# Kernel tuning notes

Hardware: AMD Instinct MI355X
Metric: run time of the kernel (lower is better)

Reference implementation:

```python
import jax, jax.numpy as jnp
import numpy as np

B, SEQ, DIM = 2, 4096, 1024
E, S = 8, 512          # num_slots = seq_len // num_experts
HID = 4 * DIM          # FeedForward hidden: dim * mult
SCALE = DIM ** 0.5     # RMSNorm scale


def rmsnorm(x, gamma):
    # matches F.normalize(x, dim=-1) * dim**0.5 * gamma (eps=1e-12 clamp on the norm)
    n = jnp.linalg.norm(x, axis=-1, keepdims=True)
    return x / jnp.maximum(n, 1e-12) * SCALE * gamma


def setup_inputs() -> dict:
    key = jax.random.key(0)
    ks = jax.random.split(key, 4)
    w_init = lambda k, shape: jax.random.normal(k, shape, dtype=jnp.float32) * 0.02
    return {
        "x": jax.random.normal(ks[0], (B, SEQ, DIM), dtype=jnp.float32),
        "norm_gamma": jnp.ones((DIM,), jnp.float32),
        "slot_norm_gamma": jnp.ones((DIM,), jnp.float32),
        "slot_embeds": jax.random.normal(ks[1], (E, S, DIM), dtype=jnp.float32),
        "w1": w_init(ks[2], (E, DIM, HID)),
        "b1": jnp.zeros((E, HID), jnp.float32),
        "w2": w_init(ks[3], (E, HID, DIM)),
        "b2": jnp.zeros((E, DIM), jnp.float32),
    }


def reference(x, norm_gamma, slot_norm_gamma, slot_embeds, w1, b1, w2, b2):
    xn = rmsnorm(x, norm_gamma)                 # [b, n, d]
    sn = rmsnorm(slot_embeds, slot_norm_gamma)  # [e, s, d]

    logits = jnp.einsum('bnd,esd->bnes', xn, sn)                   # [b, n, e, s]
    dispatch = jax.nn.softmax(logits, axis=1)                      # softmax over tokens n
    b, n, e, s = logits.shape
    combine = jax.nn.softmax(logits.reshape(b, n, e * s), axis=-1) # softmax over (e s)

    slots = jnp.einsum('bnd,bnes->besd', xn, dispatch)             # [b, e, s, d]

    # per-expert FeedForward: Linear -> GELU(exact) -> Linear (dropout=0)
    h = jnp.einsum('besd,edh->besh', slots, w1) + b1[None, :, None, :]
    h = jax.nn.gelu(h, approximate=False)
    eo = jnp.einsum('besh,ehd->besd', h, w2) + b2[None, :, None, :]

    eo = eo.reshape(b, e * s, DIM)                                 # [b, (e s), d]
    out = jnp.einsum('bmd,bnm->bnd', eo, combine)                  # [b, n, d]
    return out
```

## Files before the change

kernel.cpp:

```cpp
#include <hip/hip_runtime.h>
#include <math.h>

#define SEQ    4096
#define DIM    1024
#define NEXP   8
#define NSLOT  512
#define ES     4096
#define HID    4096
#define NB     2
#define RMS_SCALE 32.0f

typedef __attribute__((ext_vector_type(4))) float f32x4;
typedef __attribute__((ext_vector_type(8))) short bf16x8;
typedef __attribute__((ext_vector_type(4))) unsigned short us4;

__device__ __forceinline__ unsigned short f2bf(float f) {
    unsigned u = __float_as_uint(f);
    u += 0x7fff + ((u >> 16) & 1);
    return (unsigned short)(u >> 16);
}
__device__ __forceinline__ float bf2f(unsigned short h) {
    return __uint_as_float(((unsigned)h) << 16);
}
__device__ __forceinline__ float gelu_exact(float x) {
    return 0.5f * x * (1.0f + erff(x * 0.70710678118654752f));
}

#define GLOAD_LDS16(gp, lp) \
    __builtin_amdgcn_global_load_lds((const __attribute__((address_space(1))) void*)(gp), \
                                     (__attribute__((address_space(3))) void*)(lp), 16, 0, 0)

__device__ __forceinline__ unsigned ldsoff(const void* p) {
    return (unsigned)(size_t)(const __attribute__((address_space(3))) void*)p;
}

#define DSR(dst, base, off) asm volatile("ds_read_b128 %0, %1 offset:" off : "=v"(dst) : "v"(base))
#define VM(n) asm volatile("s_waitcnt vmcnt(" #n ")" ::: "memory")
#define BAR __builtin_amdgcn_s_barrier()
#define SCB __builtin_amdgcn_sched_barrier(0)

#define PH_OPEN  SCB; BAR; asm volatile("s_waitcnt lgkmcnt(0)" ::: "memory"); SCB; \
                 __builtin_amdgcn_s_setprio(1);
#define PH_CLOSE __builtin_amdgcn_s_setprio(0); SCB;

template<int ORDER>
__global__ void rmsnorm_split(const float* __restrict__ in, const float* __restrict__ gamma,
                              unsigned short* __restrict__ outc) {
    int row = blockIdx.x;
    int t = threadIdx.x;
    float4 v = reinterpret_cast<const float4*>(in + (size_t)row * DIM)[t];
    float ss = v.x*v.x + v.y*v.y + v.z*v.z + v.w*v.w;
    #pragma unroll
    for (int off = 32; off >= 1; off >>= 1) ss += __shfl_down(ss, off, 64);
    __shared__ float red[4];
    if ((t & 63) == 0) red[t >> 6] = ss;
    __syncthreads();
    float inv = RMS_SCALE / fmaxf(sqrtf(red[0] + red[1] + red[2] + red[3]), 1e-12f);
    float4 g = reinterpret_cast<const float4*>(gamma)[t];
    float f[4] = {v.x*inv*g.x, v.y*inv*g.y, v.z*inv*g.z, v.w*inv*g.w};
    us4 hv, lv;
    #pragma unroll
    for (int q = 0; q < 4; ++q) {
        unsigned short h = f2bf(f[q]);
        hv[q] = h;
        lv[q] = f2bf(f[q] - bf2f(h));
    }
    unsigned short* rb = outc + (size_t)row * 3072;
    *reinterpret_cast<us4*>(&rb[t*4]) = hv;
    if (ORDER == 0) {
        *reinterpret_cast<us4*>(&rb[1024 + t*4]) = hv;
        *reinterpret_cast<us4*>(&rb[2048 + t*4]) = lv;
    } else {
        *reinterpret_cast<us4*>(&rb[1024 + t*4]) = lv;
        *reinterpret_cast<us4*>(&rb[2048 + t*4]) = hv;
    }
}

__global__ void row_reduce(const float* __restrict__ pM, const float* __restrict__ pS,
                           float* __restrict__ rmax, float* __restrict__ rinv) {
    int row = blockIdx.x * 256 + threadIdx.x;
    float m = -INFINITY, s = 0.f;
    for (int p = 0; p < 64; ++p) {
        float m2 = pM[(size_t)p*8192 + row], s2 = pS[(size_t)p*8192 + row];
        float mn = fmaxf(m, m2);
        s = s * __expf(m - mn) + s2 * __expf(m2 - mn);
        m = mn;
    }
    rmax[row] = m; rinv[row] = 1.0f / s;
}

__global__ void col_reduce(const float* __restrict__ pM, const float* __restrict__ pS,
                           float* __restrict__ cmax, float* __restrict__ cinv) {
    int col = blockIdx.x * 256 + threadIdx.x;
    int b = blockIdx.y;
    float m = -INFINITY, s = 0.f;
    for (int p = b*32; p < b*32 + 32; ++p) {
        float m2 = pM[(size_t)p*4096 + col], s2 = pS[(size_t)p*4096 + col];
        float mn = fmaxf(m, m2);
        s = s * __expf(m - mn) + s2 * __expf(m2 - mn);
        m = mn;
    }
    cmax[b*4096 + col] = m; cinv[b*4096 + col] = 1.0f / s;
}

__global__ void make_weights(const float* __restrict__ logits,
                             const float* __restrict__ cmax, const float* __restrict__ cinv,
                             const float* __restrict__ rmax, const float* __restrict__ rinv,
                             unsigned short* __restrict__ comb, unsigned short* __restrict__ dispT) {
    int b = blockIdx.z;
    const float* L = logits + (size_t)b * SEQ * ES;
    int n0 = blockIdx.y * 32, e0 = blockIdx.x * 32;
    int t = threadIdx.x;
    int r = t >> 3, c4 = (t & 7) * 4;
    __shared__ unsigned short tile[32][36];
    float4 v = *reinterpret_cast<const float4*>(&L[(size_t)(n0 + r) * ES + e0 + c4]);
    float rm = rmax[b*SEQ + n0 + r], ri = rinv[b*SEQ + n0 + r];
    float vv[4] = {v.x, v.y, v.z, v.w};
    us4 cb;
    #pragma unroll
    for (int q = 0; q < 4; ++q) {
        cb[q] = f2bf(__expf(vv[q] - rm) * ri);
        float dv = __expf(vv[q] - cmax[b*ES + e0 + c4 + q]) * cinv[b*ES + e0 + c4 + q];
        tile[c4 + q][r] = f2bf(dv);
    }
    *reinterpret_cast<us4*>(&comb[(size_t)b*SEQ*ES + (size_t)(n0 + r)*ES + e0 + c4]) = cb;
    __syncthreads();
    us4 o = *reinterpret_cast<us4*>(&tile[t >> 3][(t & 7) * 4]);
    *reinterpret_cast<us4*>(&dispT[(size_t)b*ES*SEQ + (size_t)(e0 + (t >> 3))*SEQ + n0 + (t & 7)*4]) = o;
}

__global__ void transpose_b16(const unsigned short* __restrict__ src, unsigned short* __restrict__ dst,
                              int sld, int dld, long sStride, long dStride) {
    int z = blockIdx.z;
    const unsigned short* S = src + (size_t)z * sStride;
    unsigned short* D = dst + (size_t)z * dStride;
    int r0 = blockIdx.y * 32, c0 = blockIdx.x * 32;
    int t = threadIdx.x;
    __shared__ unsigned short tile[32][36];
    us4 v = *reinterpret_cast<const us4*>(&S[(size_t)(r0 + (t>>3)) * sld + c0 + (t&7)*4]);
    #pragma unroll
    for (int q = 0; q < 4; ++q) tile[(t&7)*4 + q][t>>3] = v[q];
    __syncthreads();
    us4 o = *reinterpret_cast<us4*>(&tile[t >> 3][(t & 7) * 4]);
    *reinterpret_cast<us4*>(&D[(size_t)(c0 + (t>>3)) * dld + r0 + (t&7)*4]) = o;
}

__global__ void transpose_f32_b16(const float* __restrict__ src, unsigned short* __restrict__ dst,
                                  int sld, int dld, long sStride, long dStride) {
    int z = blockIdx.z;
    const float* S = src + (size_t)z * sStride;
    unsigned short* D = dst + (size_t)z * dStride;
    int r0 = blockIdx.y * 32, c0 = blockIdx.x * 32;
    int t = threadIdx.x;
    __shared__ unsigned short tile[32][36];
    float4 v = *reinterpret_cast<const float4*>(&S[(size_t)(r0 + (t>>3)) * sld + c0 + (t&7)*4]);
    float vv[4] = {v.x, v.y, v.z, v.w};
    #pragma unroll
    for (int q = 0; q < 4; ++q) tile[(t&7)*4 + q][t>>3] = f2bf(vv[q]);
    __syncthreads();
    us4 o = *reinterpret_cast<us4*>(&tile[t >> 3][(t & 7) * 4]);
    *reinterpret_cast<us4*>(&D[(size_t)(c0 + (t>>3)) * dld + r0 + (t&7)*4]) = o;
}

template<int EPI, int OM, int STATS>
__global__ __launch_bounds__(512, 2)
void mfma_gemm256(const unsigned short* __restrict__ A, const unsigned short* __restrict__ B,
                  void* __restrict__ Cv, const float* __restrict__ bias,
                  int N, int K, int lda, int ldb, int ldc,
                  long aStride, long bStride, long cStride, int bMod,
                  float* __restrict__ rowpM, float* __restrict__ rowpS,
                  float* __restrict__ colpM, float* __restrict__ colpS) {
    __shared__ unsigned short lds[65536];
    const int t = threadIdx.x;
    const int lane = t & 63, wave = t >> 6;
    const int wr = wave >> 2, wc = wave & 3;
    const int z = blockIdx.z, zb = z % bMod;
    const unsigned short* Ab = A + (size_t)z * aStride;
    const unsigned short* Bb = B + (size_t)zb * bStride;
    const int gx = gridDim.x;
    int flat = blockIdx.x + blockIdx.y * gx;
    const int cpx = (gx * gridDim.y) >> 3;
    flat = (flat & 7) * cpx + (flat >> 3);
    const int m0 = (flat / gx) * 256, n0 = (flat % gx) * 256;

    const int sr = t >> 3;
    const int sg = (t & 7) ^ (sr & 7);
    const unsigned short* gA = Ab + (size_t)(m0 + sr) * lda + sg * 8;
    const int srB = sr + (sr & 32);
    const unsigned short* gB = Bb + (size_t)(n0 + srB) * ldb + sg * 8;
    unsigned short* ldsw = lds + wave * 512;

    const int lr = lane & 15, lk = lane >> 4;
    const unsigned sw0 = (unsigned)(((lk)     ^ (lr & 7)) << 4);
    const unsigned sw1 = (unsigned)(((4 + lk) ^ (lr & 7)) << 4);
    const unsigned l0  = ldsoff(lds);
    const unsigned arow = (unsigned)((wr*64 + lr) * 128);
    const unsigned brow = (unsigned)((wc*32 + lr) * 128);
    const unsigned ab00 = l0 + arow + sw0,          ab10 = l0 + arow + sw1;
    const unsigned bb00 = l0 + 32768 + brow + sw0,  bb10 = l0 + 32768 + brow + sw1;
    const unsigned ab01 = ab00 + 65536, ab11 = ab10 + 65536;
    const unsigned bb01 = bb00 + 65536, bb11 = bb10 + 65536;

    #define STAGE_A(buf, half, tt) do { \
        const unsigned short* _g = gA + (size_t)((half)*64) * lda + (tt)*64; \
        unsigned short* _l = ldsw + (buf)*32768 + (half)*8192; \
        GLOAD_LDS16(_g, _l); \
        GLOAD_LDS16(_g + (size_t)128*lda, _l + 4096); } while(0)
    #define STAGE_B(buf, half, tt) do { \
        const unsigned short* _g = gB + (size_t)((half)*32) * ldb + (tt)*64; \
        unsigned short* _l = ldsw + (buf)*32768 + 16384 + (half)*8192; \
        GLOAD_LDS16(_g, _l); \
        GLOAD_LDS16(_g + (size_t)128*ldb, _l + 4096); } while(0)

    #define MFMA16(MB, CN) \
        _Pragma("unroll") \
        for (int m = 0; m < 4; ++m) { \
            _Pragma("unroll") \
            for (int n = 0; n < 2; ++n) { \
                acc[(MB)+m][(CN)+n] = __builtin_amdgcn_mfma_f32_16x16x32_bf16(a0[m], b0[(CN)+n], acc[(MB)+m][(CN)+n], 0, 0, 0); \
                acc[(MB)+m][(CN)+n] = __builtin_amdgcn_mfma_f32_16x16x32_bf16(a1[m], b1[(CN)+n], acc[(MB)+m][(CN)+n], 0, 0, 0); \
            } \
        }

    f32x4 acc[8][4] = {};
    bf16x8 a0[4], a1[4], b0[4], b1[4];
    const int NT = K / 64;

    STAGE_A(0, 0, 0); STAGE_B(0, 0, 0); STAGE_B(0, 1, 0); STAGE_A(0, 1, 0);
    STAGE_A(1, 0, 1); STAGE_B(1, 0, 1); STAGE_B(1, 1, 1);
    VM(0); BAR;

    for (int tt = 0; tt < NT; tt += 2) {
        const bool pf2 = (tt + 2 < NT);
        const bool pf3 = (tt + 3 < NT);
        DSR(a0[0], ab00, "0");    DSR(a0[1], ab00, "2048");
        DSR(a0[2], ab00, "4096"); DSR(a0[3], ab00, "6144");
        DSR(a1[0], ab10, "0");    DSR(a1[1], ab10, "2048");
        DSR(a1[2], ab10, "4096"); DSR(a1[3], ab10, "6144");
        DSR(b0[0], bb00, "0");    DSR(b0[1], bb00, "2048");
        DSR(b1[0], bb10, "0");    DSR(b1[1], bb10, "2048");
        STAGE_A(1, 1, tt+1);
        PH_OPEN MFMA16(0, 0) PH_CLOSE
        BAR;
        DSR(b0[2], bb00, "16384"); DSR(b0[3], bb00, "18432");
        DSR(b1[2], bb10, "16384"); DSR(b1[3], bb10, "18432");
        if (pf2) STAGE_A(0, 0, tt+2);
        PH_OPEN MFMA16(0, 2) PH_CLOSE
        BAR;
        DSR(a0[0], ab00, "16384"); DSR(a0[1], ab00, "18432");
        DSR(a0[2], ab00, "20480"); DSR(a0[3], ab00, "22528");
        DSR(a1[0], ab10, "16384"); DSR(a1[1], ab10, "18432");
        DSR(a1[2], ab10, "20480"); DSR(a1[3], ab10, "22528");
        if (pf2) STAGE_B(0, 0, tt+2);
        PH_OPEN MFMA16(4, 0) PH_CLOSE
        BAR;
        if (pf2) STAGE_B(0, 1, tt+2);
        PH_OPEN MFMA16(4, 2) PH_CLOSE
        if (pf2) { VM(6); } else { VM(0); }
        BAR;
        DSR(a0[0], ab01, "0");    DSR(a0[1], ab01, "2048");
        DSR(a0[2], ab01, "4096"); DSR(a0[3], ab01, "6144");
        DSR(a1[0], ab11, "0");    DSR(a1[1], ab11, "2048");
        DSR(a1[2], ab11, "4096"); DSR(a1[3], ab11, "6144");
        DSR(b0[0], bb01, "0");    DSR(b0[1], bb01, "2048");
        DSR(b1[0], bb11, "0");    DSR(b1[1], bb11, "2048");
        if (pf2) STAGE_A(0, 1, tt+2);
        PH_OPEN MFMA16(0, 0) PH_CLOSE
        BAR;
        DSR(b0[2], bb01, "16384"); DSR(b0[3], bb01, "18432");
        DSR(b1[2], bb11, "16384"); DSR(b1[3], bb11, "18432");
        if (pf3) STAGE_A(1, 0, tt+3);
        PH_OPEN MFMA16(0, 2) PH_CLOSE
        BAR;
        DSR(a0[0], ab01, "16384"); DSR(a0[1], ab01, "18432");
        DSR(a0[2], ab01, "20480"); DSR(a0[3], ab01, "22528");
        DSR(a1[0], ab11, "16384"); DSR(a1[1], ab11, "18432");
        DSR(a1[2], ab11, "20480"); DSR(a1[3], ab11, "22528");
        if (pf3) STAGE_B(1, 0, tt+3);
        PH_OPEN MFMA16(4, 0) PH_CLOSE
        BAR;
        if (pf3) STAGE_B(1, 1, tt+3);
        PH_OPEN MFMA16(4, 2) PH_CLOSE
        if (pf3) { VM(6); } else { VM(0); }
        BAR;
    }

    if (STATS) {
        #pragma unroll
        for (int f = 0; f < 8; ++f) {
            #pragma unroll
            for (int r = 0; r < 4; ++r) {
                float m = fmaxf(fmaxf(acc[f][0][r], acc[f][1][r]), fmaxf(acc[f][2][r], acc[f][3][r]));
                #pragma unroll
                for (int msk = 1; msk <= 8; msk <<= 1) m = fmaxf(m, __shfl_xor(m, msk, 64));
                float s = __expf(acc[f][0][r]-m) + __expf(acc[f][1][r]-m)
                        + __expf(acc[f][2][r]-m) + __expf(acc[f][3][r]-m);
                #pragma unroll
                for (int msk = 1; msk <= 8; msk <<= 1) s += __shfl_xor(s, msk, 64);
                if ((lane & 15) == 0) {
                    int row = m0 + wr*128 + f*16 + (lane>>4)*4 + r;
                    int slot = (n0 >> 6) + wc;
                    rowpM[(size_t)slot*8192 + row] = m;
                    rowpS[(size_t)slot*8192 + row] = s;
                }
            }
        }
        #pragma unroll
        for (int n = 0; n < 4; ++n) {
            float m = -INFINITY;
            #pragma unroll
            for (int f = 0; f < 8; ++f)
                #pragma unroll
                for (int r = 0; r < 4; ++r) m = fmaxf(m, acc[f][n][r]);
            m = fmaxf(m, __shfl_xor(m, 16, 64));
            m = fmaxf(m, __shfl_xor(m, 32, 64));
            float s = 0.f;
            #pragma unroll
            for (int f = 0; f < 8; ++f)
                #pragma unroll
                for (int r = 0; r < 4; ++r) s += __expf(acc[f][n][r] - m);
            s += __shfl_xor(s, 16, 64);
            s += __shfl_xor(s, 32, 64);
            if ((lane >> 4) == 0) {
                int col = n0 + wc*64 + n*16 + lane;
                int slot = (m0 >> 7) + wr;
                colpM[(size_t)slot*4096 + col] = m;
                colpS[(size_t)slot*4096 + col] = s;
            }
        }
    }

    const float* bz = (EPI != 0) ? bias + (size_t)zb * N : nullptr;
    long coff = (long)z * cStride;
    int rbase = (lane >> 4) * 4;
    int cbase = lane & 15;
    #pragma unroll
    for (int f = 0; f < 8; ++f) {
        #pragma unroll
        for (int n = 0; n < 4; ++n) {
            int col  = n0 + wc*64 + n*16 + cbase;
            int row0 = m0 + wr*128 + f*16 + rbase;
            float bv = (EPI != 0) ? bz[col] : 0.f;
            float vals[4];
            #pragma unroll
            for (int r = 0; r < 4; ++r) {
                float v = acc[f][n][r] + bv;
                if (EPI == 2) v = gelu_exact(v);
                vals[r] = v;
            }
            if (OM == 0) {
                float* C = (float*)Cv + coff;
                #pragma unroll
                for (int r = 0; r < 4; ++r) C[(size_t)(row0 + r) * ldc + col] = vals[r];
            } else {
                unsigned short* C = (unsigned short*)Cv + coff;
                #pragma unroll
                for (int r = 0; r < 4; ++r) C[(size_t)(row0 + r) * ldc + col] = f2bf(vals[r]);
            }
        }
    }
    #undef STAGE_A
    #undef STAGE_B
    #undef MFMA16
}

template<int EPI, int OM>
__global__ __launch_bounds__(512, 2)
void mfma_gemmX(const unsigned short* __restrict__ A, const unsigned short* __restrict__ B,
                void* __restrict__ Cv, const float* __restrict__ bias,
                int N, int K, int lda, int ldb, int ldc,
                long aStride, long bStride, long cStride, long cStrideE, int bMod) {
    __shared__ unsigned short lds[49152];
    const int t = threadIdx.x;
    const int lane = t & 63, wave = t >> 6;
    const int wr = wave >> 2, wc = wave & 3;
    const int z = blockIdx.z, zb = z % bMod;
    const unsigned short* Ab = A + (size_t)z * aStride;
    const unsigned short* Bb = B + (size_t)zb * bStride;
    const int gx = gridDim.x;
    int flat = blockIdx.x + blockIdx.y * gx;
    const int cpx = (gx * gridDim.y) >> 3;
    flat = (flat & 7) * cpx + (flat >> 3);
    const int m0 = (flat / gx) * 256, n0 = (flat % gx) * 128;

    const int sr = t >> 3;
    const int sg = (t & 7) ^ (sr & 7);
    const unsigned short* gA = Ab + (size_t)(m0 + sr) * lda + sg * 8;
    const unsigned short* gB = Bb + (size_t)(n0 + sr) * ldb + sg * 8;
    unsigned short* ldsw = lds + wave * 512;

    const int lr = lane & 15, lk = lane >> 4;
    const unsigned g0 = (unsigned)(((lk)     ^ (lr & 7)) << 4);
    const unsigned g1 = (unsigned)(((4 + lk) ^ (lr & 7)) << 4);
    const unsigned l0 = ldsoff(lds);
    const unsigned arow = (unsigned)((wr*64 + lr) * 128);
    const unsigned brow = (unsigned)((wc*32 + lr) * 128);
    const unsigned ax00 = l0 + arow + g0,          ax10 = l0 + arow + g1;
    const unsigned bx00 = l0 + 32768 + brow + g0,  bx10 = l0 + 32768 + brow + g1;
    const unsigned ax01 = ax00 + 49152, ax11 = ax10 + 49152;
    const unsigned bx01 = bx00 + 49152, bx11 = bx10 + 49152;

    #define STAGE_AX(buf, quad, tt) do { \
        const unsigned short* _g = gA + (size_t)((quad)*64) * lda + (tt)*64; \
        unsigned short* _l = ldsw + (buf)*24576 + (quad)*8192; \
        GLOAD_LDS16(_g, _l); \
        GLOAD_LDS16(_g + (size_t)128*lda, _l + 4096); } while(0)
    #define STAGE_BX(buf, tt) do { \
        const unsigned short* _g = gB + (tt)*64; \
        unsigned short* _l = ldsw + (buf)*24576 + 16384; \
        GLOAD_LDS16(_g, _l); \
        GLOAD_LDS16(_g + (size_t)64*ldb, _l + 4096); } while(0)

    #define MFMA8(MB, AR, BR) \
        _Pragma("unroll") \
        for (int m = 0; m < 4; ++m) { \
            _Pragma("unroll") \
            for (int n = 0; n < 2; ++n) { \
                acc[(MB)+m][n] = __builtin_amdgcn_mfma_f32_16x16x32_bf16(AR[m], BR[n], acc[(MB)+m][n], 0, 0, 0); \
            } \
        }

    f32x4 acc[8][2] = {};
    bf16x8 a0[4], a1[4], b0[2], b1[2];
    const int NT = K / 64;

    STAGE_AX(0, 0, 0); STAGE_BX(0, 0); STAGE_AX(0, 1, 0);
    STAGE_AX(1, 0, 1); STAGE_BX(1, 1);
    VM(0); BAR;

    for (int tt = 0; tt < NT; tt += 2) {
        const bool pf2 = (tt + 2 < NT);
        const bool pf3 = (tt + 3 < NT);
        DSR(a0[0], ax00, "0");    DSR(a0[1], ax00, "2048");
        DSR(a0[2], ax00, "4096"); DSR(a0[3], ax00, "6144");
        DSR(b0[0], bx00, "0");    DSR(b0[1], bx00, "2048");
        STAGE_AX(1, 1, tt+1);
        PH_OPEN MFMA8(0, a0, b0) PH_CLOSE
        BAR;
        DSR(a1[0], ax10, "0");    DSR(a1[1], ax10, "2048");
        DSR(a1[2], ax10, "4096"); DSR(a1[3], ax10, "6144");
        DSR(b1[0], bx10, "0");    DSR(b1[1], bx10, "2048");
        PH_OPEN MFMA8(0, a1, b1) PH_CLOSE
        BAR;
        DSR(a0[0], ax00, "16384"); DSR(a0[1], ax00, "18432");
        DSR(a0[2], ax00, "20480"); DSR(a0[3], ax00, "22528");
        if (pf2) STAGE_AX(0, 0, tt+2);
        PH_OPEN MFMA8(4, a0, b0) PH_CLOSE
        BAR;
        DSR(a1[0], ax10, "16384"); DSR(a1[1], ax10, "18432");
        DSR(a1[2], ax10, "20480"); DSR(a1[3], ax10, "22528");
        if (pf2) STAGE_BX(0, tt+2);
        PH_OPEN MFMA8(4, a1, b1) PH_CLOSE
        if (pf2) { VM(4); } else { VM(0); }
        BAR;
        DSR(a0[0], ax01, "0");    DSR(a0[1], ax01, "2048");
        DSR(a0[2], ax01, "4096"); DSR(a0[3], ax01, "6144");
        DSR(b0[0], bx01, "0");    DSR(b0[1], bx01, "2048");
        if (pf2) STAGE_AX(0, 1, tt+2);
        PH_OPEN MFMA8(0, a0, b0) PH_CLOSE
        BAR;
        DSR(a1[0], ax11, "0");    DSR(a1[1], ax11, "2048");
        DSR(a1[2], ax11, "4096"); DSR(a1[3], ax11, "6144");
        DSR(b1[0], bx11, "0");    DSR(b1[1], bx11, "2048");
        PH_OPEN MFMA8(0, a1, b1) PH_CLOSE
        BAR;
        DSR(a0[0], ax01, "16384"); DSR(a0[1], ax01, "18432");
        DSR(a0[2], ax01, "20480"); DSR(a0[3], ax01, "22528");
        if (pf3) STAGE_AX(1, 0, tt+3);
        PH_OPEN MFMA8(4, a0, b0) PH_CLOSE
        BAR;
        DSR(a1[0], ax11, "16384"); DSR(a1[1], ax11, "18432");
        DSR(a1[2], ax11, "20480"); DSR(a1[3], ax11, "22528");
        if (pf3) STAGE_BX(1, tt+3);
        PH_OPEN MFMA8(4, a1, b1) PH_CLOSE
        if (pf3) { VM(4); } else { VM(0); }
        BAR;
    }

    const float* bz = (EPI != 0) ? bias + (size_t)zb * N : nullptr;
    long coff = (long)z * cStride + (long)zb * cStrideE;
    int rbase = (lane >> 4) * 4;
    int cbase = lane & 15;
    #pragma unroll
    for (int f = 0; f < 8; ++f) {
        #pragma unroll
        for (int n = 0; n < 2; ++n) {
            int col  = n0 + wc*32 + n*16 + cbase;
            int row0 = m0 + wr*128 + f*16 + rbase;
            float bv = (EPI != 0) ? bz[col] : 0.f;
            float vals[4];
            #pragma unroll
            for (int r = 0; r < 4; ++r) {
                float v = acc[f][n][r] + bv;
                if (EPI == 2) v = gelu_exact(v);
                vals[r] = v;
            }
            if (OM == 0) {
                float* C = (float*)Cv + coff;
                #pragma unroll
                for (int r = 0; r < 4; ++r) C[(size_t)(row0 + r) * ldc + col] = vals[r];
            } else if (OM == 1) {
                unsigned short* C = (unsigned short*)Cv + coff;
                #pragma unroll
                for (int r = 0; r < 4; ++r) C[(size_t)(row0 + r) * ldc + col] = f2bf(vals[r]);
            } else {
                unsigned short* C = (unsigned short*)Cv + coff;
                us4 o;
                #pragma unroll
                for (int r = 0; r < 4; ++r) o[r] = f2bf(vals[r]);
                *reinterpret_cast<us4*>(&C[(size_t)col * ldc + row0]) = o;
            }
        }
    }
    #undef STAGE_AX
    #undef STAGE_BX
    #undef MFMA8
}

extern "C" void kernel_launch(void* const* d_in, const int* in_sizes, int n_in,
                              void* d_out, int out_size, void* d_ws, size_t ws_size,
                              hipStream_t stream) {
    const float* x    = (const float*)d_in[0];
    const float* ng   = (const float*)d_in[1];
    const float* sg   = (const float*)d_in[2];
    const float* semb = (const float*)d_in[3];
    const float* w1   = (const float*)d_in[4];
    const float* b1   = (const float*)d_in[5];
    const float* w2   = (const float*)d_in[6];
    const float* b2   = (const float*)d_in[7];
    float* out = (float*)d_out;

    char* base = (char*)d_ws;
    unsigned short* Acat  = (unsigned short*)(base);
    unsigned short* Bcat  = (unsigned short*)(base + 50331648);
    unsigned short* dispT = (unsigned short*)(base);
    unsigned short* w2T   = (unsigned short*)(base);
    float*          logits= (float*)(base + 75497472);
    unsigned short* hbuf  = (unsigned short*)(base + 75497472);
    unsigned short* w1T   = (unsigned short*)(base + 142606336);
    unsigned short* xnT   = (unsigned short*)(base + 209715200);
    unsigned short* comb  = (unsigned short*)(base + 226492416);
    unsigned short* slots = (unsigned short*)(base + 293601280);
    unsigned short* eoT   = (unsigned short*)(base + 293601280);
    float* rowpM = (float*)(base + 226492416);
    float* rowpS = rowpM + 64*8192;
    float* colpM = rowpS + 64*8192;
    float* colpS = colpM + 64*4096;
    float* cmax = (float*)(base + 310378496);
    float* cinv = cmax + 8192;
    float* rmax = cinv + 8192;
    float* rinv = rmax + 8192;

    rmsnorm_split<0><<<NB*SEQ, 256, 0, stream>>>(x, ng, Acat);
    rmsnorm_split<1><<<NEXP*NSLOT, 256, 0, stream>>>(semb, sg, Bcat);

    transpose_b16<<<dim3(DIM/32, SEQ/32, NB), 256, 0, stream>>>(
        Acat, xnT, 3072, SEQ, (long)SEQ*3072, (long)DIM*SEQ);

    mfma_gemm256<0,0,1><<<dim3(ES/256, (NB*SEQ)/256, 1), 512, 0, stream>>>(
        Acat, Bcat, logits, nullptr, ES, 3072, 3072, 3072, ES,
        0L, 0L, 0L, 1, rowpM, rowpS, colpM, colpS);

    row_reduce<<<32, 256, 0, stream>>>(rowpM, rowpS, rmax, rinv);
    col_reduce<<<dim3(16, 2), 256, 0, stream>>>(colpM, colpS, cmax, cinv);

    make_weights<<<dim3(ES/32, SEQ/32, NB), 256, 0, stream>>>(
        logits, cmax, cinv, rmax, rinv, comb, dispT);

    transpose_f32_b16<<<dim3(HID/32, DIM/32, NEXP), 256, 0, stream>>>(
        w1, w1T, HID, DIM, (long)DIM*HID, (long)HID*DIM);

    mfma_gemmX<0,1><<<dim3(DIM/128, ES/256, NB), 512, 0, stream>>>(
        dispT, xnT, slots, nullptr, DIM, SEQ, SEQ, SEQ, DIM,
        (long)ES*SEQ, (long)DIM*SEQ, (long)ES*DIM, 0L, NB);

    transpose_f32_b16<<<dim3(DIM/32, HID/32, NEXP), 256, 0, stream>>>(
        w2, w2T, DIM, HID, (long)HID*DIM, (long)DIM*HID);

    mfma_gemm256<2,1,0><<<dim3(HID/256, NSLOT/256, NB*NEXP), 512, 0, stream>>>(
        slots, w1T, hbuf, b1, HID, DIM, DIM, DIM, HID,
        (long)NSLOT*DIM, (long)HID*DIM, (long)NSLOT*HID, NEXP,
        nullptr, nullptr, nullptr, nullptr);

    mfma_gemmX<1,2><<<dim3(DIM/128, NSLOT/256, NB*NEXP), 512, 0, stream>>>(
        hbuf, w2T, eoT, b2, DIM, HID, HID, HID, ES,
        (long)NSLOT*HID, (long)DIM*HID, (long)(DIM*ES/NEXP), (long)(NSLOT - DIM*ES/NEXP), NEXP);

    mfma_gemmX<0,0><<<dim3(DIM/128, SEQ/256, NB), 512, 0, stream>>>(
        comb, eoT, out, nullptr, DIM, ES, ES, ES, DIM,
        (long)SEQ*ES, (long)DIM*ES, (long)SEQ*DIM, 0L, NB);
}
```

Measured before the change: 694.4 us.

## Defer softmax normalization to GEMM epilogues and compact split-bf16 operand storage

The logits GEMM epilogue now computes only the partial row and column maxes, not the exp-sums. The unnormalized exponentials are summed in make_weights, reduced by new sum kernels, and applied as per-row scales in the dispatch and combine GEMM epilogues. This removes the exp work from the large GEMM epilogue. Separately, the split-bf16 hi/lo operands are stored once (2048 columns) instead of being duplicated (3072), with the GEMM index-wrapping the K offsets to form the same three-term product. This reduces staging writes and footprint, but adds two small launches and extra reduction traffic.

```diff
diff --git a/kernel.cpp b/kernel.cpp
--- a/kernel.cpp
+++ b/kernel.cpp
@@ -43,7 +43,6 @@
                  __builtin_amdgcn_s_setprio(1);
 #define PH_CLOSE __builtin_amdgcn_s_setprio(0); SCB;
 
-template<int ORDER>
 __global__ void rmsnorm_split(const float* __restrict__ in, const float* __restrict__ gamma,
                               unsigned short* __restrict__ outc) {
     int row = blockIdx.x;
@@ -65,48 +64,35 @@
         hv[q] = h;
         lv[q] = f2bf(f[q] - bf2f(h));
     }
-    unsigned short* rb = outc + (size_t)row * 3072;
+    unsigned short* rb = outc + (size_t)row * 2048;
     *reinterpret_cast<us4*>(&rb[t*4]) = hv;
-    if (ORDER == 0) {
-        *reinterpret_cast<us4*>(&rb[1024 + t*4]) = hv;
-        *reinterpret_cast<us4*>(&rb[2048 + t*4]) = lv;
-    } else {
-        *reinterpret_cast<us4*>(&rb[1024 + t*4]) = lv;
-        *reinterpret_cast<us4*>(&rb[2048 + t*4]) = hv;
-    }
-}
-
-__global__ void row_reduce(const float* __restrict__ pM, const float* __restrict__ pS,
-                           float* __restrict__ rmax, float* __restrict__ rinv) {
+    *reinterpret_cast<us4*>(&rb[1024 + t*4]) = lv;
+}
+
+__global__ void rowmax_reduce(const float* __restrict__ pM, float* __restrict__ rmax) {
     int row = blockIdx.x * 256 + threadIdx.x;
-    float m = -INFINITY, s = 0.f;
-    for (int p = 0; p < 64; ++p) {
-        float m2 = pM[(size_t)p*8192 + row], s2 = pS[(size_t)p*8192 + row];
-        float mn = fmaxf(m, m2);
-        s = s * __expf(m - mn) + s2 * __expf(m2 - mn);
-        m = mn;
-    }
-    rmax[row] = m; rinv[row] = 1.0f / s;
-}
-
-__global__ void col_reduce(const float* __restrict__ pM, const float* __restrict__ pS,
-                           float* __restrict__ cmax, float* __restrict__ cinv) {
+    float m = -INFINITY;
+    for (int p = 0; p < 64; ++p) m = fmaxf(m, pM[(size_t)p*8192 + row]);
+    rmax[row] = m;
+}
+__global__ void colmax_reduce(const float* __restrict__ pM, float* __restrict__ cmax) {
     int col = blockIdx.x * 256 + threadIdx.x;
     int b = blockIdx.y;
-    float m = -INFINITY, s = 0.f;
-    for (int p = b*32; p < b*32 + 32; ++p) {
-        float m2 = pM[(size_t)p*4096 + col], s2 = pS[(size_t)p*4096 + col];
-        float mn = fmaxf(m, m2);
-        s = s * __expf(m - mn) + s2 * __expf(m2 - mn);
-        m = mn;
-    }
-    cmax[b*4096 + col] = m; cinv[b*4096 + col] = 1.0f / s;
+    float m = -INFINITY;
+    for (int p = b*32; p < b*32 + 32; ++p) m = fmaxf(m, pM[(size_t)p*4096 + col]);
+    cmax[b*4096 + col] = m;
+}
+__global__ void sum_reduce(const float* __restrict__ pS, float* __restrict__ sinv) {
+    int fl = blockIdx.x * 256 + threadIdx.x;
+    float s = 0.f;
+    for (int p = 0; p < 128; ++p) s += pS[(size_t)p*8192 + fl];
+    sinv[fl] = 1.0f / s;
 }
 
 __global__ void make_weights(const float* __restrict__ logits,
-                             const float* __restrict__ cmax, const float* __restrict__ cinv,
-                             const float* __restrict__ rmax, const float* __restrict__ rinv,
-                             unsigned short* __restrict__ comb, unsigned short* __restrict__ dispT) {
+                             const float* __restrict__ cmax, const float* __restrict__ rmax,
+                             unsigned short* __restrict__ comb, unsigned short* __restrict__ dispT,
+                             float* __restrict__ rowpS, float* __restrict__ colpS) {
     int b = blockIdx.z;
     const float* L = logits + (size_t)b * SEQ * ES;
     int n0 = blockIdx.y * 32, e0 = blockIdx.x * 32;
@@ -114,19 +100,32 @@
     int r = t >> 3, c4 = (t & 7) * 4;
     __shared__ unsigned short tile[32][36];
     float4 v = *reinterpret_cast<const float4*>(&L[(size_t)(n0 + r) * ES + e0 + c4]);
-    float rm = rmax[b*SEQ + n0 + r], ri = rinv[b*SEQ + n0 + r];
+    float rm = rmax[b*SEQ + n0 + r];
     float vv[4] = {v.x, v.y, v.z, v.w};
     us4 cb;
+    float rs = 0.f;
     #pragma unroll
     for (int q = 0; q < 4; ++q) {
-        cb[q] = f2bf(__expf(vv[q] - rm) * ri);
-        float dv = __expf(vv[q] - cmax[b*ES + e0 + c4 + q]) * cinv[b*ES + e0 + c4 + q];
+        cb[q] = f2bf(__expf(vv[q] - rm));
+        rs += bf2f(cb[q]);
+        float dv = __expf(vv[q] - cmax[b*ES + e0 + c4 + q]);
         tile[c4 + q][r] = f2bf(dv);
     }
     *reinterpret_cast<us4*>(&comb[(size_t)b*SEQ*ES + (size_t)(n0 + r)*ES + e0 + c4]) = cb;
+    rs += __shfl_xor(rs, 1, 64);
+    rs += __shfl_xor(rs, 2, 64);
+    rs += __shfl_xor(rs, 4, 64);
+    if ((t & 7) == 0)
+        rowpS[(size_t)blockIdx.x * 8192 + b*SEQ + n0 + r] = rs;
     __syncthreads();
     us4 o = *reinterpret_cast<us4*>(&tile[t >> 3][(t & 7) * 4]);
     *reinterpret_cast<us4*>(&dispT[(size_t)b*ES*SEQ + (size_t)(e0 + (t >> 3))*SEQ + n0 + (t & 7)*4]) = o;
+    float cs = bf2f(o[0]) + bf2f(o[1]) + bf2f(o[2]) + bf2f(o[3]);
+    cs += __shfl_xor(cs, 1, 64);
+    cs += __shfl_xor(cs, 2, 64);
+    cs += __shfl_xor(cs, 4, 64);
+    if ((t & 7) == 0)
+        colpS[(size_t)blockIdx.y * 8192 + b*ES + e0 + (t >> 3)] = cs;
 }
 
 __global__ void transpose_b16(const unsigned short* __restrict__ src, unsigned short* __restrict__ dst,
@@ -162,14 +161,13 @@
     *reinterpret_cast<us4*>(&D[(size_t)(c0 + (t>>3)) * dld + r0 + (t&7)*4]) = o;
 }
 
-template<int EPI, int OM, int STATS>
+template<int EPI, int OM, int STATS, int SPLIT>
 __global__ __launch_bounds__(512, 2)
 void mfma_gemm256(const unsigned short* __restrict__ A, const unsigned short* __restrict__ B,
                   void* __restrict__ Cv, const float* __restrict__ bias,
                   int N, int K, int lda, int ldb, int ldc,
                   long aStride, long bStride, long cStride, int bMod,
-                  float* __restrict__ rowpM, float* __restrict__ rowpS,
-                  float* __restrict__ colpM, float* __restrict__ colpS) {
+                  float* __restrict__ rowpM, float* __restrict__ colpM) {
     __shared__ unsigned short lds[65536];
     const int t = threadIdx.x;
     const int lane = t & 63, wave = t >> 6;
@@ -201,13 +199,16 @@
     const unsigned ab01 = ab00 + 65536, ab11 = ab10 + 65536;
     const unsigned bb01 = bb00 + 65536, bb11 = bb10 + 65536;
 
+    #define KOA(tt) ((size_t)((SPLIT && (tt) >= 16) ? ((tt)-16)*64 : (tt)*64))
+    #define KOB(tt) ((size_t)((SPLIT && (tt) >= 32) ? ((tt)-32)*64 : (tt)*64))
+
     #define STAGE_A(buf, half, tt) do { \
-        const unsigned short* _g = gA + (size_t)((half)*64) * lda + (tt)*64; \
+        const unsigned short* _g = gA + (size_t)((half)*64) * lda + KOA(tt); \
         unsigned short* _l = ldsw + (buf)*32768 + (half)*8192; \
         GLOAD_LDS16(_g, _l); \
         GLOAD_LDS16(_g + (size_t)128*lda, _l + 4096); } while(0)
     #define STAGE_B(buf, half, tt) do { \
-        const unsigned short* _g = gB + (size_t)((half)*32) * ldb + (tt)*64; \
+        const unsigned short* _g = gB + (size_t)((half)*32) * ldb + KOB(tt); \
         unsigned short* _l = ldsw + (buf)*32768 + 16384 + (half)*8192; \
         GLOAD_LDS16(_g, _l); \
         GLOAD_LDS16(_g + (size_t)128*ldb, _l + 4096); } while(0)
@@ -293,15 +294,10 @@
                 float m = fmaxf(fmaxf(acc[f][0][r], acc[f][1][r]), fmaxf(acc[f][2][r], acc[f][3][r]));
                 #pragma unroll
                 for (int msk = 1; msk <= 8; msk <<= 1) m = fmaxf(m, __shfl_xor(m, msk, 64));
-                float s = __expf(acc[f][0][r]-m) + __expf(acc[f][1][r]-m)
-                        + __expf(acc[f][2][r]-m) + __expf(acc[f][3][r]-m);
-                #pragma unroll
-                for (int msk = 1; msk <= 8; msk <<= 1) s += __shfl_xor(s, msk, 64);
                 if ((lane & 15) == 0) {
                     int row = m0 + wr*128 + f*16 + (lane>>4)*4 + r;
                     int slot = (n0 >> 6) + wc;
                     rowpM[(size_t)slot*8192 + row] = m;
-                    rowpS[(size_t)slot*8192 + row] = s;
                 }
             }
         }
@@ -314,18 +310,10 @@
                 for (int r = 0; r < 4; ++r) m = fmaxf(m, acc[f][n][r]);
             m = fmaxf(m, __shfl_xor(m, 16, 64));
             m = fmaxf(m, __shfl_xor(m, 32, 64));
-            float s = 0.f;
-            #pragma unroll
-            for (int f = 0; f < 8; ++f)
-                #pragma unroll
-                for (int r = 0; r < 4; ++r) s += __expf(acc[f][n][r] - m);
-            s += __shfl_xor(s, 16, 64);
-            s += __shfl_xor(s, 32, 64);
             if ((lane >> 4) == 0) {
                 int col = n0 + wc*64 + n*16 + lane;
                 int slot = (m0 >> 7) + wr;
                 colpM[(size_t)slot*4096 + col] = m;
-                colpS[(size_t)slot*4096 + col] = s;
             }
         }
     }
@@ -362,14 +350,17 @@
     #undef STAGE_A
     #undef STAGE_B
     #undef MFMA16
-}
-
-template<int EPI, int OM>
+    #undef KOA
+    #undef KOB
+}
+
+template<int EPI, int OM, int SC>
 __global__ __launch_bounds__(512, 2)
 void mfma_gemmX(const unsigned short* __restrict__ A, const unsigned short* __restrict__ B,
                 void* __restrict__ Cv, const float* __restrict__ bias,
                 int N, int K, int lda, int ldb, int ldc,
-                long aStride, long bStride, long cStride, long cStrideE, int bMod) {
+                long aStride, long bStride, long cStride, long cStrideE, int bMod,
+                const float* __restrict__ svec) {
     __shared__ unsigned short lds[49152];
     const int t = threadIdx.x;
     const int lane = t & 63, wave = t >> 6;
@@ -478,6 +469,7 @@
     }
 
     const float* bz = (EPI != 0) ? bias + (size_t)zb * N : nullptr;
+    const float* sv = SC ? svec + (size_t)z * 4096 : nullptr;
     long coff = (long)z * cStride + (long)zb * cStrideE;
     int rbase = (lane >> 4) * 4;
     int cbase = lane & 15;
@@ -492,6 +484,7 @@
             #pragma unroll
             for (int r = 0; r < 4; ++r) {
                 float v = acc[f][n][r] + bv;
+                if (SC) v *= sv[row0 + r];
                 if (EPI == 2) v = gelu_exact(v);
                 vals[r] = v;
             }
@@ -532,7 +525,7 @@
 
     char* base = (char*)d_ws;
     unsigned short* Acat  = (unsigned short*)(base);
-    unsigned short* Bcat  = (unsigned short*)(base + 50331648);
+    unsigned short* Bcat  = (unsigned short*)(base + 33554432);
     unsigned short* dispT = (unsigned short*)(base);
     unsigned short* w2T   = (unsigned short*)(base);
     float*          logits= (float*)(base + 75497472);
@@ -543,50 +536,54 @@
     unsigned short* slots = (unsigned short*)(base + 293601280);
     unsigned short* eoT   = (unsigned short*)(base + 293601280);
     float* rowpM = (float*)(base + 226492416);
-    float* rowpS = rowpM + 64*8192;
-    float* colpM = rowpS + 64*8192;
-    float* colpS = colpM + 64*4096;
-    float* cmax = (float*)(base + 310378496);
-    float* cinv = cmax + 8192;
-    float* rmax = cinv + 8192;
-    float* rinv = rmax + 8192;
-
-    rmsnorm_split<0><<<NB*SEQ, 256, 0, stream>>>(x, ng, Acat);
-    rmsnorm_split<1><<<NEXP*NSLOT, 256, 0, stream>>>(semb, sg, Bcat);
+    float* colpM = rowpM + 64*8192;
+    float* rmax  = (float*)(base + 310378496);
+    float* rinv  = rmax + 8192;
+    float* cmax  = rinv + 8192;
+    float* cinv  = cmax + 8192;
+    float* rowpS = cinv + 8192;
+    float* colpS = rowpS + 128*8192;
+
+    rmsnorm_split<<<NB*SEQ, 256, 0, stream>>>(x, ng, Acat);
+    rmsnorm_split<<<NEXP*NSLOT, 256, 0, stream>>>(semb, sg, Bcat);
 
     transpose_b16<<<dim3(DIM/32, SEQ/32, NB), 256, 0, stream>>>(
-        Acat, xnT, 3072, SEQ, (long)SEQ*3072, (long)DIM*SEQ);
-
-    mfma_gemm256<0,0,1><<<dim3(ES/256, (NB*SEQ)/256, 1), 512, 0, stream>>>(
-        Acat, Bcat, logits, nullptr, ES, 3072, 3072, 3072, ES,
-        0L, 0L, 0L, 1, rowpM, rowpS, colpM, colpS);
-
-    row_reduce<<<32, 256, 0, stream>>>(rowpM, rowpS, rmax, rinv);
-    col_reduce<<<dim3(16, 2), 256, 0, stream>>>(colpM, colpS, cmax, cinv);
+        Acat, xnT, 2048, SEQ, (long)SEQ*2048, (long)DIM*SEQ);
+
+    mfma_gemm256<0,0,1,1><<<dim3(ES/256, (NB*SEQ)/256, 1), 512, 0, stream>>>(
+        Acat, Bcat, logits, nullptr, ES, 3072, 2048, 2048, ES,
+        0L, 0L, 0L, 1, rowpM, colpM);
+
+    rowmax_reduce<<<32, 256, 0, stream>>>(rowpM, rmax);
+    colmax_reduce<<<dim3(16, 2), 256, 0, stream>>>(colpM, cmax);
 
     make_weights<<<dim3(ES/32, SEQ/32, NB), 256, 0, stream>>>(
-        logits, cmax, cinv, rmax, rinv, comb, dispT);
+        logits, cmax, rmax, comb, dispT, rowpS, colpS);
+
+    sum_reduce<<<32, 256, 0, stream>>>(rowpS, rinv);
+    sum_reduce<<<32, 256, 0, stream>>>(colpS, cinv);
 
     transpose_f32_b16<<<dim3(HID/32, DIM/32, NEXP), 256, 0, stream>>>(
         w1, w1T, HID, DIM, (long)DIM*HID, (long)HID*DIM);
 
-    mfma_gemmX<0,1><<<dim3(DIM/128, ES/256, NB), 512, 0, stream>>>(
+    mfma_gemmX<0,1,1><<<dim3(DIM/128, ES/256, NB), 512, 0, stream>>>(
         dispT, xnT, slots, nullptr, DIM, SEQ, SEQ, SEQ, DIM,
-        (long)ES*SEQ, (long)DIM*SEQ, (long)ES*DIM, 0L, NB);
+        (long)ES*SEQ, (long)DIM*SEQ, (long)ES*DIM, 0L, NB, cinv);
 
     transpose_f32_b16<<<dim3(DIM/32, HID/32, NEXP), 256, 0, stream>>>(
         w2, w2T, DIM, HID, (long)HID*DIM, (long)DIM*HID);
 
-    mfma_gemm256<2,1,0><<<dim3(HID/256, NSLOT/256, NB*NEXP), 512, 0, stream>>>(
+    mfma_gemm256<2,1,0,0><<<dim3(HID/256, NSLOT/256, NB*NEXP), 512, 0, stream>>>(
         slots, w1T, hbuf, b1, HID, DIM, DIM, DIM, HID,
         (long)NSLOT*DIM, (long)HID*DIM, (long)NSLOT*HID, NEXP,
-        nullptr, nullptr, nullptr, nullptr);
-
-    mfma_gemmX<1,2><<<dim3(DIM/128, NSLOT/256, NB*NEXP), 512, 0, stream>>>(
+        nullptr, nullptr);
+
+    mfma_gemmX<1,2,0><<<dim3(DIM/128, NSLOT/256, NB*NEXP), 512, 0, stream>>>(
         hbuf, w2T, eoT, b2, DIM, HID, HID, HID, ES,
-        (long)NSLOT*HID, (long)DIM*HID, (long)(DIM*ES/NEXP), (long)(NSLOT - DIM*ES/NEXP), NEXP);
-
-    mfma_gemmX<0,0><<<dim3(DIM/128, SEQ/256, NB), 512, 0, stream>>>(
+        (long)NSLOT*HID, (long)DIM*HID, (long)(DIM*ES/NEXP), (long)(NSLOT - DIM*ES/NEXP), NEXP,
+        nullptr);
+
+    mfma_gemmX<0,0,1><<<dim3(DIM/128, SEQ/256, NB), 512, 0, stream>>>(
         comb, eoT, out, nullptr, DIM, ES, ES, ES, DIM,
-        (long)SEQ*ES, (long)DIM*ES, (long)SEQ*DIM, 0L, NB);
-}
+        (long)SEQ*ES, (long)DIM*ES, (long)SEQ*DIM, 0L, NB, rinv);
+}
```

Result: no change. 700.7 us (+0.9%).
